# Kernel optimization log

Hardware: AMD Instinct MI355X
Metric: run time of the kernel (lower is better)

Reference implementation:

```python
import jax, jax.numpy as jnp
import numpy as np

B, S, D = 4, 2048, 1024
O = 1024
E = 8
K = 2

def setup_inputs() -> dict:
    key = jax.random.key(0)
    k1, k2, k3, k4, k5 = jax.random.split(key, 5)
    scale = 1.0 / np.sqrt(D)
    x = jax.random.normal(k1, (B, S, D), dtype=jnp.float32)
    # expert linear layers stacked: weight [E, D, O], bias [E, O]
    We = jax.random.uniform(k2, (E, D, O), dtype=jnp.float32, minval=-scale, maxval=scale)
    be = jax.random.uniform(k3, (E, O), dtype=jnp.float32, minval=-scale, maxval=scale)
    # gate linear: weight [D, E], bias [E]
    Wg = jax.random.uniform(k4, (D, E), dtype=jnp.float32, minval=-scale, maxval=scale)
    bg = jax.random.uniform(k5, (E,), dtype=jnp.float32, minval=-scale, maxval=scale)
    return {"x": x, "We": We, "be": be, "Wg": Wg, "bg": bg}

def reference(x, We, be, Wg, bg):
    b, s, d = x.shape
    x_flat = x.reshape(-1, d)                                   # [N, D]
    gates = jax.nn.softmax(x_flat @ Wg + bg, axis=-1)           # [N, E]
    topk_gates, topk_idx = jax.lax.top_k(gates, K)              # [N, K]
    topk_gates = topk_gates / jnp.sum(topk_gates, axis=1, keepdims=True)
    # dense all-expert compute (faithful to original naive MoE)
    expert_out = jnp.einsum('nd,edo->neo', x_flat, We) + be     # [N, E, O]
    # gather top-k expert outputs per token
    selected = jnp.take_along_axis(expert_out, topk_idx[:, :, None], axis=1)  # [N, K, O]
    out = jnp.sum(selected * topk_gates[:, :, None], axis=1)    # [N, O]
    return out.reshape(b, s, -1)
```

## Files before the change

### kernel.cpp

```cpp
#include <hip/hip_runtime.h>

#define N_TOK 8192
#define DDIM 1024
#define ODIM 1024
#define NEXP 8

typedef __attribute__((ext_vector_type(8))) short bf16x8;
typedef __attribute__((ext_vector_type(4))) float f32x4;

__device__ __forceinline__ unsigned int f2bf(float f) {
    unsigned int u = __float_as_uint(f);
    return (u + 0x7fffu + ((u >> 16) & 1u)) >> 16;
}
__device__ __forceinline__ float bflo(unsigned int u) { return __uint_as_float(u << 16); }
__device__ __forceinline__ float bfhi(unsigned int u) { return __uint_as_float(u & 0xffff0000u); }

__device__ __forceinline__ void async_copy16(const unsigned short* g, unsigned short* l) {
    __builtin_amdgcn_global_load_lds(
        (const __attribute__((address_space(1))) unsigned int*)g,
        (__attribute__((address_space(3))) unsigned int*)l, 16, 0, 0);
}

__global__ __launch_bounds__(256) void prep_kernel(const float* __restrict__ x,
                                                   const float* __restrict__ Wg,
                                                   const float* __restrict__ bg,
                                                   const float* __restrict__ We,
                                                   int* __restrict__ ea, int* __restrict__ eb,
                                                   float* __restrict__ ga, float* __restrict__ gb,
                                                   unsigned short* __restrict__ xbf,
                                                   unsigned short* __restrict__ WeT,
                                                   int* __restrict__ counts) {
    __shared__ float tile[64][65];
    if (blockIdx.x < 2048) {
        if (blockIdx.x == 0) counts[threadIdx.x] = 0;
        const int wave = threadIdx.x >> 6, lane = threadIdx.x & 63;
        const int t = blockIdx.x * 4 + wave;
        const float* xr = x + (size_t)t * DDIM;

        float4 v[4];
#pragma unroll
        for (int c = 0; c < 4; ++c) v[c] = *(const float4*)&xr[c * 256 + lane * 4];

        unsigned short* xo = xbf + (size_t)t * DDIM;
#pragma unroll
        for (int c = 0; c < 4; ++c) {
            uint2 w;
            w.x = f2bf(v[c].x) | (f2bf(v[c].y) << 16);
            w.y = f2bf(v[c].z) | (f2bf(v[c].w) << 16);
            *(uint2*)&xo[c * 256 + lane * 4] = w;
        }

        float acc[8] = {0, 0, 0, 0, 0, 0, 0, 0};
#pragma unroll
        for (int c = 0; c < 4; ++c) {
            const int dbase = c * 256 + lane * 4;
#pragma unroll
            for (int j = 0; j < 4; ++j) {
                float xv = ((const float*)&v[c])[j];
                const float4* w = (const float4*)(Wg + (size_t)(dbase + j) * 8);
                float4 w0 = w[0], w1 = w[1];
                acc[0] += xv * w0.x; acc[1] += xv * w0.y; acc[2] += xv * w0.z; acc[3] += xv * w0.w;
                acc[4] += xv * w1.x; acc[5] += xv * w1.y; acc[6] += xv * w1.z; acc[7] += xv * w1.w;
            }
        }
#pragma unroll
        for (int off = 32; off > 0; off >>= 1) {
#pragma unroll
            for (int j = 0; j < 8; ++j) acc[j] += __shfl_xor(acc[j], off, 64);
        }
        if (lane == 0) {
            float s[8];
#pragma unroll
            for (int e = 0; e < 8; ++e) s[e] = acc[e] + bg[e];
            int a = 0;
#pragma unroll
            for (int e = 1; e < 8; ++e) if (s[e] > s[a]) a = e;
            int b = (a == 0) ? 1 : 0;
#pragma unroll
            for (int e = 0; e < 8; ++e) if (e != a && e != b && s[e] > s[b]) b = e;
            float g0 = 1.0f / (1.0f + __expf(s[b] - s[a]));
            ea[t] = a; eb[t] = b; ga[t] = g0; gb[t] = 1.0f - g0;
        }
    } else {
        const int lin = blockIdx.x - 2048;
        const int e = lin >> 8, rem = lin & 255;
        const int d0 = (rem >> 4) * 64, o0 = (rem & 15) * 64;
        const int tid = threadIdx.x;
#pragma unroll
        for (int p = 0; p < 4; ++p) {
            int idx = p * 256 + tid;
            int row = idx >> 4, c = idx & 15;
            float4 v = *(const float4*)&We[(((size_t)e * 1024 + d0 + row) << 10) + o0 + (c << 2)];
            tile[row][c * 4 + 0] = v.x; tile[row][c * 4 + 1] = v.y;
            tile[row][c * 4 + 2] = v.z; tile[row][c * 4 + 3] = v.w;
        }
        __syncthreads();
#pragma unroll
        for (int p = 0; p < 2; ++p) {
            int idx = p * 256 + tid;
            int orow = idx >> 3, c8 = idx & 7;
            unsigned int u[8];
#pragma unroll
            for (int j = 0; j < 8; ++j) u[j] = f2bf(tile[c8 * 8 + j][orow]);
            uint4 q;
            q.x = u[0] | (u[1] << 16); q.y = u[2] | (u[3] << 16);
            q.z = u[4] | (u[5] << 16); q.w = u[6] | (u[7] << 16);
            *(uint4*)&WeT[(((size_t)e * 1024 + o0 + orow) << 10) + d0 + (c8 << 3)] = q;
        }
    }
}

__global__ __launch_bounds__(64) void scatter_kernel(const int* __restrict__ ea,
                                                     const int* __restrict__ eb,
                                                     int* __restrict__ counts,
                                                     int* __restrict__ btok,
                                                     int* __restrict__ slotA,
                                                     int* __restrict__ slotB) {
    const int t = blockIdx.x * 64 + threadIdx.x;
    const int lane = threadIdx.x & 63;
#pragma unroll
    for (int pass = 0; pass < 2; ++pass) {
        const int e = (pass == 0) ? ea[t] : eb[t];
        int* slot = (pass == 0) ? slotA : slotB;
#pragma unroll
        for (int ex = 0; ex < NEXP; ++ex) {
            unsigned long long mask = __ballot(e == ex);
            if (mask) {
                int leader = __ffsll((long long)mask) - 1;
                int base = 0;
                if (lane == leader) base = atomicAdd(&counts[ex * 32], __popcll(mask));
                base = __shfl(base, leader, 64);
                if (e == ex) {
                    int pos = base + __popcll(mask & ((1ull << lane) - 1ull));
                    btok[ex * N_TOK + pos] = t;
                    slot[t] = ex * N_TOK + pos;
                }
            }
        }
    }
}

__global__ __launch_bounds__(256) void moe_gemm(const unsigned short* __restrict__ xbf,
                                                const unsigned short* __restrict__ WeT,
                                                const float* __restrict__ be,
                                                const int* __restrict__ counts,
                                                const int* __restrict__ btok,
                                                unsigned short* __restrict__ ybuf) {
    const int id = blockIdx.x;
    const int e = id & 7;
    const int n0 = ((id >> 3) & 7) * 128;
    const int r0 = (id >> 6) * 128;
    const int cnt = counts[e * 32];
    if (r0 >= cnt) return;

    __shared__ unsigned short sA[128 * 64];
    __shared__ unsigned short sB[128 * 64];
    __shared__ int s_tok[128];

    const int tid = threadIdx.x;
    if (tid < 128) {
        int r = r0 + tid;
        int rc = (r < cnt) ? r : (cnt - 1);
        s_tok[tid] = btok[e * N_TOK + rc];
    }
    const int wave = tid >> 6, lane = tid & 63;
    __syncthreads();

    const int colo = (((lane & 7) ^ (lane >> 3)) * 8);
    size_t a_off[4];
    size_t b_off[4];
#pragma unroll
    for (int p = 0; p < 4; ++p) {
        int row = wave * 32 + p * 8 + (lane >> 3);
        a_off[p] = ((size_t)s_tok[row] << 10) + colo;
        b_off[p] = (((size_t)e * 1024 + n0 + row) << 10) + colo;
    }

    const int wm = (wave >> 1) * 64, wn = (wave & 1) * 64;
    const int quad = lane >> 4, rA = lane & 15;
    const int sw = rA & 7;

    f32x4 acc[4][4];
#pragma unroll
    for (int mi = 0; mi < 4; ++mi)
#pragma unroll
        for (int ni = 0; ni < 4; ++ni) acc[mi][ni] = (f32x4){0.f, 0.f, 0.f, 0.f};

    for (int kb = 0; kb < DDIM; kb += 64) {
#pragma unroll
        for (int p = 0; p < 4; ++p) {
            unsigned short* la = &sA[(wave * 32 + p * 8) * 64];
            unsigned short* lb = &sB[(wave * 32 + p * 8) * 64];
            async_copy16(xbf + a_off[p] + kb, la);
            async_copy16(WeT + b_off[p] + kb, lb);
        }
        __syncthreads();
#pragma unroll
        for (int ks = 0; ks < 2; ++ks) {
            const int cslot = ((ks * 4 + quad) ^ sw) * 8;
            bf16x8 af[4], bfr[4];
#pragma unroll
            for (int mi = 0; mi < 4; ++mi)
                af[mi] = *(bf16x8*)&sA[(wm + mi * 16 + rA) * 64 + cslot];
#pragma unroll
            for (int ni = 0; ni < 4; ++ni)
                bfr[ni] = *(bf16x8*)&sB[(wn + ni * 16 + rA) * 64 + cslot];
#pragma unroll
            for (int mi = 0; mi < 4; ++mi)
#pragma unroll
                for (int ni = 0; ni < 4; ++ni)
                    acc[mi][ni] = __builtin_amdgcn_mfma_f32_16x16x32_bf16(af[mi], bfr[ni], acc[mi][ni], 0, 0, 0);
        }
        __syncthreads();
    }

#pragma unroll
    for (int ni = 0; ni < 4; ++ni) {
        int col = n0 + wn + ni * 16 + rA;
        float bias = be[(e << 10) + col];
#pragma unroll
        for (int mi = 0; mi < 4; ++mi) {
#pragma unroll
            for (int r = 0; r < 4; ++r) {
                int lrow = wm + mi * 16 + quad * 4 + r;
                if (r0 + lrow < cnt) {
                    ybuf[(((size_t)e * N_TOK + r0 + lrow) << 10) + col] =
                        (unsigned short)f2bf(acc[mi][ni][r] + bias);
                }
            }
        }
    }
}

__global__ __launch_bounds__(256) void combine_kernel(const unsigned short* __restrict__ ybuf,
                                                      const int* __restrict__ slotA,
                                                      const int* __restrict__ slotB,
                                                      const float* __restrict__ ga,
                                                      const float* __restrict__ gb,
                                                      float* __restrict__ out) {
    const int wave = threadIdx.x >> 6, lane = threadIdx.x & 63;
    const int t = blockIdx.x * 4 + wave;
    const unsigned short* ra = ybuf + ((size_t)slotA[t] << 10);
    const unsigned short* rb = ybuf + ((size_t)slotB[t] << 10);
    const float a = ga[t], b = gb[t];
    float* orow = out + ((size_t)t << 10);
#pragma unroll
    for (int i = 0; i < 2; ++i) {
        int c = i * 512 + lane * 8;
        uint4 ua = *(const uint4*)&ra[c];
        uint4 ub = *(const uint4*)&rb[c];
        float4 o0, o1;
        o0.x = a * bflo(ua.x) + b * bflo(ub.x);
        o0.y = a * bfhi(ua.x) + b * bfhi(ub.x);
        o0.z = a * bflo(ua.y) + b * bflo(ub.y);
        o0.w = a * bfhi(ua.y) + b * bfhi(ub.y);
        o1.x = a * bflo(ua.z) + b * bflo(ub.z);
        o1.y = a * bfhi(ua.z) + b * bfhi(ub.z);
        o1.z = a * bflo(ua.w) + b * bflo(ub.w);
        o1.w = a * bfhi(ua.w) + b * bfhi(ub.w);
        *(float4*)&orow[c] = o0;
        *(float4*)&orow[c + 4] = o1;
    }
}

extern "C" void kernel_launch(void* const* d_in, const int* in_sizes, int n_in,
                              void* d_out, int out_size, void* d_ws, size_t ws_size,
                              hipStream_t stream) {
    const float* x  = (const float*)d_in[0];
    const float* We = (const float*)d_in[1];
    const float* be = (const float*)d_in[2];
    const float* Wg = (const float*)d_in[3];
    const float* bg = (const float*)d_in[4];
    float* out = (float*)d_out;

    char* ws = (char*)d_ws;
    size_t off = 0;
    int* counts = (int*)(ws + off); off += 8 * 32 * 4;
    int* btok   = (int*)(ws + off); off += NEXP * N_TOK * 4;
    int* slotA  = (int*)(ws + off); off += N_TOK * 4;
    int* slotB  = (int*)(ws + off); off += N_TOK * 4;
    int* ea = (int*)(ws + off); off += N_TOK * 4;
    int* eb = (int*)(ws + off); off += N_TOK * 4;
    float* ga = (float*)(ws + off); off += N_TOK * 4;
    float* gb = (float*)(ws + off); off += N_TOK * 4;
    unsigned short* WeT  = (unsigned short*)(ws + off); off += (size_t)NEXP * DDIM * ODIM * 2;
    unsigned short* xbf  = (unsigned short*)(ws + off); off += (size_t)N_TOK * DDIM * 2;
    unsigned short* ybuf = (unsigned short*)(ws + off); off += (size_t)NEXP * N_TOK * ODIM * 2;

    prep_kernel<<<dim3(4096), 256, 0, stream>>>(x, Wg, bg, We, ea, eb, ga, gb, xbf, WeT, counts);
    scatter_kernel<<<dim3(N_TOK / 64), 64, 0, stream>>>(ea, eb, counts, btok, slotA, slotB);
    moe_gemm<<<dim3(64 * 8 * 8), 256, 0, stream>>>(xbf, WeT, be, counts, btok, ybuf);
    combine_kernel<<<dim3(N_TOK / 4), 256, 0, stream>>>(ybuf, slotA, slotB, ga, gb, out);
}
```

Before: 234.1 us.

## Enlarge MoE GEMM tiles to 256x256 with double-buffered LDS prefetch

The grouped expert GEMM now uses 256x256 output tiles computed by 512-thread blocks, with 8x4 MFMA accumulators per wave. The A and B LDS buffers are double-buffered, so the async global-to-LDS loads for the next K slice are issued before the current slice's MFMAs, which removes one barrier per iteration. Offsets are switched to 32-bit arithmetic. The goals are better data reuse per tile and overlap of loads with compute. The costs are higher register pressure, 128KB of LDS per block, and more padded rows wasted on experts whose token count is not a multiple of 256.

```diff
diff --git a/kernel.cpp b/kernel.cpp
--- a/kernel.cpp
+++ b/kernel.cpp
@@ -140,78 +140,87 @@
     }
 }
 
-__global__ __launch_bounds__(256) void moe_gemm(const unsigned short* __restrict__ xbf,
-                                                const unsigned short* __restrict__ WeT,
-                                                const float* __restrict__ be,
-                                                const int* __restrict__ counts,
-                                                const int* __restrict__ btok,
-                                                unsigned short* __restrict__ ybuf) {
+__global__ __launch_bounds__(512, 2) void moe_gemm(const unsigned short* __restrict__ xbf,
+                                                   const unsigned short* __restrict__ WeT,
+                                                   const float* __restrict__ be,
+                                                   const int* __restrict__ counts,
+                                                   const int* __restrict__ btok,
+                                                   unsigned short* __restrict__ ybuf) {
     const int id = blockIdx.x;
     const int e = id & 7;
-    const int n0 = ((id >> 3) & 7) * 128;
-    const int r0 = (id >> 6) * 128;
+    const int n0 = ((id >> 3) & 3) * 256;
+    const int r0 = (id >> 5) * 256;
     const int cnt = counts[e * 32];
     if (r0 >= cnt) return;
 
-    __shared__ unsigned short sA[128 * 64];
-    __shared__ unsigned short sB[128 * 64];
-    __shared__ int s_tok[128];
+    __shared__ unsigned short sA[2][256 * 64];
+    __shared__ unsigned short sB[2][256 * 64];
+    __shared__ int s_tok[256];
 
     const int tid = threadIdx.x;
-    if (tid < 128) {
+    if (tid < 256) {
         int r = r0 + tid;
         int rc = (r < cnt) ? r : (cnt - 1);
         s_tok[tid] = btok[e * N_TOK + rc];
     }
-    const int wave = tid >> 6, lane = tid & 63;
+    const int w = tid >> 6, lane = tid & 63;
     __syncthreads();
 
-    const int colo = (((lane & 7) ^ (lane >> 3)) * 8);
-    size_t a_off[4];
-    size_t b_off[4];
+    const int rsub = lane >> 3;
+    const int colo = ((lane & 7) ^ rsub) * 8;
+    unsigned int a_off[4], b_off[4];
 #pragma unroll
     for (int p = 0; p < 4; ++p) {
-        int row = wave * 32 + p * 8 + (lane >> 3);
-        a_off[p] = ((size_t)s_tok[row] << 10) + colo;
-        b_off[p] = (((size_t)e * 1024 + n0 + row) << 10) + colo;
-    }
-
-    const int wm = (wave >> 1) * 64, wn = (wave & 1) * 64;
+        int row = p * 64 + w * 8 + rsub;
+        a_off[p] = ((unsigned)s_tok[row] << 10) + colo;
+        b_off[p] = ((unsigned)(e * 1024 + n0 + row) << 10) + colo;
+    }
+
+    const int wm = (w >> 2) * 128, wn = (w & 3) * 64;
     const int quad = lane >> 4, rA = lane & 15;
     const int sw = rA & 7;
 
-    f32x4 acc[4][4];
-#pragma unroll
-    for (int mi = 0; mi < 4; ++mi)
+    f32x4 acc[8][4];
+#pragma unroll
+    for (int mi = 0; mi < 8; ++mi)
 #pragma unroll
         for (int ni = 0; ni < 4; ++ni) acc[mi][ni] = (f32x4){0.f, 0.f, 0.f, 0.f};
 
-    for (int kb = 0; kb < DDIM; kb += 64) {
-#pragma unroll
-        for (int p = 0; p < 4; ++p) {
-            unsigned short* la = &sA[(wave * 32 + p * 8) * 64];
-            unsigned short* lb = &sB[(wave * 32 + p * 8) * 64];
-            async_copy16(xbf + a_off[p] + kb, la);
-            async_copy16(WeT + b_off[p] + kb, lb);
-        }
-        __syncthreads();
+#pragma unroll
+    for (int p = 0; p < 4; ++p) {
+        async_copy16(xbf + a_off[p], &sA[0][(p * 64 + w * 8) * 64]);
+        async_copy16(WeT + b_off[p], &sB[0][(p * 64 + w * 8) * 64]);
+    }
+    __syncthreads();
+
+    int buf = 0;
+    for (int kb = 0; kb < 16; ++kb) {
+        if (kb < 15) {
+            const int ko = (kb + 1) * 64;
+            const int nb = buf ^ 1;
+#pragma unroll
+            for (int p = 0; p < 4; ++p) {
+                async_copy16(xbf + a_off[p] + ko, &sA[nb][(p * 64 + w * 8) * 64]);
+                async_copy16(WeT + b_off[p] + ko, &sB[nb][(p * 64 + w * 8) * 64]);
+            }
+        }
 #pragma unroll
         for (int ks = 0; ks < 2; ++ks) {
             const int cslot = ((ks * 4 + quad) ^ sw) * 8;
-            bf16x8 af[4], bfr[4];
-#pragma unroll
-            for (int mi = 0; mi < 4; ++mi)
-                af[mi] = *(bf16x8*)&sA[(wm + mi * 16 + rA) * 64 + cslot];
+            bf16x8 bfr[4];
 #pragma unroll
             for (int ni = 0; ni < 4; ++ni)
-                bfr[ni] = *(bf16x8*)&sB[(wn + ni * 16 + rA) * 64 + cslot];
-#pragma unroll
-            for (int mi = 0; mi < 4; ++mi)
+                bfr[ni] = *(bf16x8*)&sB[buf][(wn + ni * 16 + rA) * 64 + cslot];
+#pragma unroll
+            for (int mi = 0; mi < 8; ++mi) {
+                bf16x8 af = *(bf16x8*)&sA[buf][(wm + mi * 16 + rA) * 64 + cslot];
 #pragma unroll
                 for (int ni = 0; ni < 4; ++ni)
-                    acc[mi][ni] = __builtin_amdgcn_mfma_f32_16x16x32_bf16(af[mi], bfr[ni], acc[mi][ni], 0, 0, 0);
+                    acc[mi][ni] = __builtin_amdgcn_mfma_f32_16x16x32_bf16(af, bfr[ni], acc[mi][ni], 0, 0, 0);
+            }
         }
         __syncthreads();
+        buf ^= 1;
     }
 
 #pragma unroll
@@ -219,12 +228,12 @@
         int col = n0 + wn + ni * 16 + rA;
         float bias = be[(e << 10) + col];
 #pragma unroll
-        for (int mi = 0; mi < 4; ++mi) {
+        for (int mi = 0; mi < 8; ++mi) {
 #pragma unroll
             for (int r = 0; r < 4; ++r) {
                 int lrow = wm + mi * 16 + quad * 4 + r;
                 if (r0 + lrow < cnt) {
-                    ybuf[(((size_t)e * N_TOK + r0 + lrow) << 10) + col] =
+                    ybuf[(((size_t)(e * N_TOK + r0 + lrow)) << 10) + col] =
                         (unsigned short)f2bf(acc[mi][ni][r] + bias);
                 }
             }
@@ -289,6 +298,6 @@
 
     prep_kernel<<<dim3(4096), 256, 0, stream>>>(x, Wg, bg, We, ea, eb, ga, gb, xbf, WeT, counts);
     scatter_kernel<<<dim3(N_TOK / 64), 64, 0, stream>>>(ea, eb, counts, btok, slotA, slotB);
-    moe_gemm<<<dim3(64 * 8 * 8), 256, 0, stream>>>(xbf, WeT, be, counts, btok, ybuf);
+    moe_gemm<<<dim3(32 * 4 * 8), 512, 0, stream>>>(xbf, WeT, be, counts, btok, ybuf);
     combine_kernel<<<dim3(N_TOK / 4), 256, 0, stream>>>(ybuf, slotA, slotB, ga, gb, out);
 }
```

Result: slower. 247.3 us (+5.6%).
